# Kernel optimization log

Hardware: AMD Instinct MI355X
Metric: run time of the kernel (lower is better)

The kernel has to match this reference:

```python
import jax, jax.numpy as jnp
import numpy as np

N_NODES = 100000
N_EDGES = 1600000
IN_F, HID, OUT_F = 50, 256, 121


def setup_inputs() -> dict:
    key = jax.random.key(0)
    ks = jax.random.split(key, 8)
    x = jax.random.normal(ks[0], (N_NODES, IN_F), dtype=jnp.float32)
    edge_index = jax.random.randint(ks[1], (2, N_EDGES), 0, N_NODES, dtype=jnp.int64)
    W1 = jax.random.normal(ks[2], (IN_F, HID), dtype=jnp.float32) * (1.0 / np.sqrt(IN_F))
    b1 = jnp.zeros((HID,), dtype=jnp.float32)
    W2 = jax.random.normal(ks[3], (HID, HID), dtype=jnp.float32) * (1.0 / np.sqrt(HID))
    b2 = jnp.zeros((HID,), dtype=jnp.float32)
    W3 = jax.random.normal(ks[4], (HID, OUT_F), dtype=jnp.float32) * (1.0 / np.sqrt(HID))
    b3 = jnp.zeros((OUT_F,), dtype=jnp.float32)
    return {"x": x, "edge_index": edge_index, "W1": W1, "b1": b1,
            "W2": W2, "b2": b2, "W3": W3, "b3": b3}


def _gcn_norm(edge_index, num_nodes):
    # PyG gcn_norm: add self-loops, symmetric degree normalization.
    loop = jnp.arange(num_nodes, dtype=edge_index.dtype)
    row = jnp.concatenate([edge_index[0], loop])  # source
    col = jnp.concatenate([edge_index[1], loop])  # target (aggregation dim)
    ones = jnp.ones(row.shape[0], dtype=jnp.float32)
    deg = jax.ops.segment_sum(ones, col, num_segments=num_nodes)
    dinv = jnp.where(deg > 0, jax.lax.rsqrt(deg), 0.0)
    norm = dinv[row] * dinv[col]  # [E+N]
    return row, col, norm


def _gcn_conv(x, W, b, row, col, norm, num_nodes):
    h = x @ W                                   # [N, F_out] dense transform
    msg = h[row] * norm[:, None]                # gather + scale  [E+N, F_out]
    agg = jax.ops.segment_sum(msg, col, num_segments=num_nodes)  # scatter-add
    return agg + b


def reference(x, edge_index, W1, b1, W2, b2, W3, b3):
    n = x.shape[0]
    row, col, norm = _gcn_norm(edge_index, n)
    # layer 1 + relu (dropout is identity in eval mode)
    x1 = _gcn_conv(x, W1, b1, row, col, norm, n)
    h = jax.nn.relu(x1)
    # layer 2 + relu
    x1 = _gcn_conv(h, W2, b2, row, col, norm, n)
    h = jax.nn.relu(x1)
    # layer 3; module returns pre-relu output x1 of the last conv
    x1 = _gcn_conv(h, W3, b3, row, col, norm, n)
    return x1
```

## Files before the change

### kernel.cpp

```cpp
#include <hip/hip_runtime.h>


#define IN_F 50
#define HID  256
#define OUT_F 121
#define KP1  64
#define NP3  128
#define MPAD 100096

typedef __attribute__((ext_vector_type(8))) short bf16x8;
typedef __attribute__((ext_vector_type(4))) float f32x4;

__device__ __forceinline__ float bf2f(unsigned short u) {
    union { unsigned int i; float f; } x; x.i = ((unsigned int)u) << 16; return x.f;
}
__device__ __forceinline__ unsigned short f2bf(float f) {
    union { float f; unsigned int i; } x; x.f = f;
    unsigned int r = x.i + 0x7FFFu + ((x.i >> 16) & 1u);
    return (unsigned short)(r >> 16);
}

__device__ __forceinline__ void gl2lds16(const void* g, void* l) {
    __builtin_amdgcn_global_load_lds(
        (const __attribute__((address_space(1))) void*)g,
        (__attribute__((address_space(3))) void*)l, 16, 0, 0);
}

__global__ void k_detect(const int* __restrict__ ei, int* __restrict__ flag, int N) {
    int i = threadIdx.x;
    int lo = ei[2 * i], hi = ei[2 * i + 1];
    int bad = (hi != 0) || ((unsigned)lo >= (unsigned)N);
    unsigned long long m = __ballot(bad);
    if (threadIdx.x == 0) *flag = (m == 0ULL) ? 1 : 0;
}


__global__ void k_count(const int* __restrict__ ei, const int* __restrict__ flag,
                        int* __restrict__ cnt, int E, int N) {
    int t = blockIdx.x * blockDim.x + threadIdx.x;
    if (t >= E) return;
    int f = *flag;
    int c = f ? ei[2 * (E + t)] : ei[E + t];
    c = min(max(c, 0), N - 1);
    atomicAdd(&cnt[c], 1);
}

__global__ __launch_bounds__(1024) void k_scan(const int* __restrict__ cnt,
                                               int* __restrict__ offs,
                                               float* __restrict__ dinv, int n) {
    __shared__ int wsum[16];
    __shared__ int s_carry;
    int lane = threadIdx.x & 63, wid = threadIdx.x >> 6;
    if (threadIdx.x == 0) s_carry = 0;
    __syncthreads();
    for (int base = 0; base < n; base += 4096) {
        int i0 = base + (int)threadIdx.x * 4;
        int v0 = (i0 + 0 < n) ? cnt[i0 + 0] : 0;
        int v1 = (i0 + 1 < n) ? cnt[i0 + 1] : 0;
        int v2 = (i0 + 2 < n) ? cnt[i0 + 2] : 0;
        int v3 = (i0 + 3 < n) ? cnt[i0 + 3] : 0;
        int s1 = v0 + v1, s2 = s1 + v2, tsum = s2 + v3;
        int x = tsum;
        #pragma unroll
        for (int d = 1; d < 64; d <<= 1) {
            int y = __shfl_up(x, d, 64);
            if (lane >= d) x += y;
        }
        if (lane == 63) wsum[wid] = x;
        __syncthreads();
        int wpre = 0;
        #pragma unroll
        for (int j = 0; j < 16; j++) wpre += (j < wid) ? wsum[j] : 0;
        int carry = s_carry;
        int e0 = carry + wpre + x - tsum;
        if (i0 + 0 < n) { offs[i0+0]=e0;    dinv[i0+0]=rsqrtf((float)(v0+1)); }
        if (i0 + 1 < n) { offs[i0+1]=e0+v0; dinv[i0+1]=rsqrtf((float)(v1+1)); }
        if (i0 + 2 < n) { offs[i0+2]=e0+s1; dinv[i0+2]=rsqrtf((float)(v2+1)); }
        if (i0 + 3 < n) { offs[i0+3]=e0+s2; dinv[i0+3]=rsqrtf((float)(v3+1)); }
        __syncthreads();
        if (threadIdx.x == 1023) s_carry = carry + wpre + x;
        __syncthreads();
    }
    if (threadIdx.x == 0) offs[n] = s_carry;
}

__global__ void k_fill(const int* __restrict__ ei, const int* __restrict__ flag,
                       const int* __restrict__ offs,
                       int* __restrict__ fillc, int* __restrict__ rowidx, int E, int N) {
    int t = blockIdx.x * blockDim.x + threadIdx.x;
    if (t >= E) return;
    int f = *flag;
    int c = f ? ei[2 * (E + t)] : ei[E + t];
    int r = f ? ei[2 * t] : ei[t];
    c = min(max(c, 0), N - 1);
    r = min(max(r, 0), N - 1);
    int pos = offs[c] + atomicAdd(&fillc[c], 1);
    if ((unsigned)pos < (unsigned)E) rowidx[pos] = r;
}


__global__ void k_padx(const float* __restrict__ x, const float* __restrict__ dinv,
                       unsigned short* __restrict__ Xs, int N) {
    int idx = blockIdx.x * blockDim.x + threadIdx.x;
    if (idx >= N * KP1) return;
    int node = idx >> 6, k = idx & 63;
    Xs[idx] = (k < IN_F) ? f2bf(dinv[node] * x[node * IN_F + k]) : (unsigned short)0;
}

__global__ void k_tr(const float* __restrict__ W, unsigned short* __restrict__ Bt,
                     int K, int Nw, int Kp, int Np) {
    int idx = blockIdx.x * blockDim.x + threadIdx.x;
    if (idx >= Np * Kp) return;
    int nn = idx / Kp, k = idx - nn * Kp;
    Bt[idx] = (k < K && nn < Nw) ? f2bf(W[k * Nw + nn]) : (unsigned short)0;
}

__global__ __launch_bounds__(256) void k_gemm_lds(const unsigned short* __restrict__ A,
                                                  const unsigned short* __restrict__ Bt,
                                                  const float* __restrict__ dinv,
                                                  const float* __restrict__ bias,
                                                  unsigned short* __restrict__ C,
                                                  int K, int Nout,
                                                  int BIAS, int RELU, int SCALE) {
    __shared__ char lds[16384];
    const int tid = threadIdx.x;
    const int wid = tid >> 6, lane = tid & 63;
    const int wm = wid & 1, wn = wid >> 1;
    const int quad = lane >> 4, ml = lane & 15;
    const int m0 = blockIdx.x * 128;
    const int n0g = blockIdx.y * 128;

    f32x4 acc[4][4];
    #pragma unroll
    for (int a = 0; a < 4; a++)
        #pragma unroll
        for (int b = 0; b < 4; b++) acc[a][b] = (f32x4){0.f, 0.f, 0.f, 0.f};

    for (int kk = 0; kk < K; kk += 32) {
        #pragma unroll
        for (int r = 0; r < 2; r++) {
            int c = r * 256 + tid;
            int row = c >> 2, q = c & 3;
            gl2lds16(A  + (size_t)(m0  + row) * K + kk + q * 8, lds + c * 16);
            gl2lds16(Bt + (size_t)(n0g + row) * K + kk + q * 8, lds + 8192 + c * 16);
        }
        __syncthreads();
        bf16x8 af[4], bfv[4];
        #pragma unroll
        for (int mf = 0; mf < 4; mf++)
            af[mf] = *(const bf16x8*)(lds + ((wm * 64 + mf * 16 + ml) * 64 + quad * 16));
        #pragma unroll
        for (int nf = 0; nf < 4; nf++)
            bfv[nf] = *(const bf16x8*)(lds + 8192 + ((wn * 64 + nf * 16 + ml) * 64 + quad * 16));
        #pragma unroll
        for (int mf = 0; mf < 4; mf++)
            #pragma unroll
            for (int nf = 0; nf < 4; nf++)
                acc[mf][nf] = __builtin_amdgcn_mfma_f32_16x16x32_bf16(af[mf], bfv[nf], acc[mf][nf], 0, 0, 0);
        __syncthreads();
    }

    #pragma unroll
    for (int mf = 0; mf < 4; mf++) {
        int r0 = m0 + wm * 64 + mf * 16 + quad * 4;
        float dd[4] = {1.f, 1.f, 1.f, 1.f};
        if (SCALE) { dd[0]=dinv[r0]; dd[1]=dinv[r0+1]; dd[2]=dinv[r0+2]; dd[3]=dinv[r0+3]; }
        #pragma unroll
        for (int nf = 0; nf < 4; nf++) {
            int col = n0g + wn * 64 + nf * 16 + ml;
            float bb = BIAS ? bias[col] : 0.f;
            #pragma unroll
            for (int i = 0; i < 4; i++) {
                float v = acc[mf][nf][i] + bb;
                if (RELU) v = fmaxf(v, 0.f);
                v *= dd[i];
                C[(size_t)(r0 + i) * Nout + col] = f2bf(v);
            }
        }
    }
}


__device__ __forceinline__ int rclamp(int r, int N) { return min(max(r, 0), N - 1); }

__global__ void k_aggx(const unsigned short* __restrict__ Xs,
                       const int* __restrict__ offs, const int* __restrict__ rowidx,
                       const float* __restrict__ dinv, unsigned short* __restrict__ Y, int N) {
    int wid = threadIdx.x >> 6, lane = threadIdx.x & 63;
    int sub = lane >> 3, sl = lane & 7;
    int node = blockIdx.x * 32 + wid * 8 + sub;
    int nc = min(node, N - 1);
    int c = sl * 8;
    bf16x8 s = *(const bf16x8*)(Xs + (size_t)nc * KP1 + c);
    float a[8];
    #pragma unroll
    for (int k = 0; k < 8; k++) a[k] = bf2f((unsigned short)s[k]);
    int e = offs[nc], end = offs[nc + 1];
    if (node >= N) { e = 0; end = 0; }
    while (__any(e < end)) {
        int r[4]; float m[4];
        #pragma unroll
        for (int j = 0; j < 4; j++) {
            int idx = e + j;
            m[j] = (idx < end) ? 1.f : 0.f;
            idx = min(idx, end - 1); idx = max(idx, 0);
            r[j] = rclamp(rowidx[idx], N);
        }
        bf16x8 u[4];
        #pragma unroll
        for (int j = 0; j < 4; j++)
            u[j] = *(const bf16x8*)(Xs + (size_t)r[j] * KP1 + c);
        #pragma unroll
        for (int j = 0; j < 4; j++)
            #pragma unroll
            for (int k = 0; k < 8; k++)
                a[k] = fmaf(bf2f((unsigned short)u[j][k]), m[j], a[k]);
        e += 4;
    }
    if (node < N) {
        float dv = dinv[node];
        bf16x8 o;
        #pragma unroll
        for (int k = 0; k < 8; k++) o[k] = (short)f2bf(a[k] * dv);
        *(bf16x8*)(Y + (size_t)node * KP1 + c) = o;
    }
}

__global__ void k_agg256s(const unsigned short* __restrict__ Hn,
                          const int* __restrict__ offs, const int* __restrict__ rowidx,
                          const float* __restrict__ dinv, unsigned short* __restrict__ Y,
                          int N, int half_n) {
    int cell = blockIdx.x & 7;
    int chunk = cell >> 1, half = cell & 1;
    int idx = blockIdx.x >> 3;
    int wid = threadIdx.x >> 6, lane = threadIdx.x & 63;
    int sub = lane >> 3, sl = lane & 7;
    int node = half * half_n + idx * 32 + wid * 8 + sub;
    int hi_end = min((half + 1) * half_n, N);
    int ok = node < hi_end;
    int nc = ok ? node : hi_end - 1;
    int c = chunk * 64 + sl * 8;
    bf16x8 s = *(const bf16x8*)(Hn + (size_t)nc * HID + c);
    float a[8];
    #pragma unroll
    for (int k = 0; k < 8; k++) a[k] = bf2f((unsigned short)s[k]);
    int e = offs[nc], end = offs[nc + 1];
    if (!ok) { e = 0; end = 0; }
    while (__any(e < end)) {
        int r[4]; float m[4];
        #pragma unroll
        for (int j = 0; j < 4; j++) {
            int idx2 = e + j;
            m[j] = (idx2 < end) ? 1.f : 0.f;
            idx2 = min(idx2, end - 1); idx2 = max(idx2, 0);
            r[j] = rclamp(rowidx[idx2], N);
        }
        bf16x8 u[4];
        #pragma unroll
        for (int j = 0; j < 4; j++)
            u[j] = *(const bf16x8*)(Hn + (size_t)r[j] * HID + c);
        #pragma unroll
        for (int j = 0; j < 4; j++)
            #pragma unroll
            for (int k = 0; k < 8; k++)
                a[k] = fmaf(bf2f((unsigned short)u[j][k]), m[j], a[k]);
        e += 4;
    }
    if (ok) {
        float dv = dinv[node];
        bf16x8 o;
        #pragma unroll
        for (int k = 0; k < 8; k++) o[k] = (short)f2bf(a[k] * dv);
        *(bf16x8*)(Y + (size_t)node * HID + c) = o;
    }
}

__global__ void k_aggouts(const unsigned short* __restrict__ G,
                          const int* __restrict__ offs, const int* __restrict__ rowidx,
                          const float* __restrict__ dinv, const float* __restrict__ bias,
                          float* __restrict__ out, int N, int quar_n) {
    int cell = blockIdx.x & 7;
    int chunk = cell >> 2, quar = cell & 3;
    int idx = blockIdx.x >> 3;
    int wid = threadIdx.x >> 6, lane = threadIdx.x & 63;
    int sub = lane >> 3, sl = lane & 7;
    int node = quar * quar_n + idx * 32 + wid * 8 + sub;
    int hi_end = min((quar + 1) * quar_n, N);
    int ok = node < hi_end;
    int nc = ok ? node : hi_end - 1;
    int c = chunk * 64 + sl * 8;
    bf16x8 s = *(const bf16x8*)(G + (size_t)nc * NP3 + c);
    float a[8];
    #pragma unroll
    for (int k = 0; k < 8; k++) a[k] = bf2f((unsigned short)s[k]);
    int e = offs[nc], end = offs[nc + 1];
    if (!ok) { e = 0; end = 0; }
    while (__any(e < end)) {
        int r[4]; float m[4];
        #pragma unroll
        for (int j = 0; j < 4; j++) {
            int idx2 = e + j;
            m[j] = (idx2 < end) ? 1.f : 0.f;
            idx2 = min(idx2, end - 1); idx2 = max(idx2, 0);
            r[j] = rclamp(rowidx[idx2], N);
        }
        bf16x8 u[4];
        #pragma unroll
        for (int j = 0; j < 4; j++)
            u[j] = *(const bf16x8*)(G + (size_t)r[j] * NP3 + c);
        #pragma unroll
        for (int j = 0; j < 4; j++)
            #pragma unroll
            for (int k = 0; k < 8; k++)
                a[k] = fmaf(bf2f((unsigned short)u[j][k]), m[j], a[k]);
        e += 4;
    }
    if (ok) {
        float dv = dinv[node];
        #pragma unroll
        for (int k = 0; k < 8; k++) {
            int col = c + k;
            if (col < OUT_F)
                out[(size_t)node * OUT_F + col] = fmaf(a[k], dv, bias[col]);
        }
    }
}


extern "C" void kernel_launch(void* const* d_in, const int* in_sizes, int n_in,
                              void* d_out, int out_size, void* d_ws, size_t ws_size,
                              hipStream_t stream) {
    const float* x  = (const float*)d_in[0];
    const int*   ei = (const int*)d_in[1];
    const float* W1 = (const float*)d_in[2];
    const float* b1 = (const float*)d_in[3];
    const float* W2 = (const float*)d_in[4];
    const float* b2 = (const float*)d_in[5];
    const float* W3 = (const float*)d_in[6];
    const float* b3 = (const float*)d_in[7];
    float* out = (float*)d_out;

    const int N = in_sizes[0] / IN_F;
    const int E = in_sizes[1] / 2;

    char* w = (char*)d_ws;
    size_t off = 0;
    auto alloc = [&](size_t bytes) -> char* {
        char* p = w + off;
        off += (bytes + 255) & ~(size_t)255;
        return p;
    };
    int*   cnt    = (int*)  alloc((size_t)N * 4);
    int*   offs   = (int*)  alloc((size_t)(N + 1) * 4);
    int*   fillc  = (int*)  alloc((size_t)N * 4);
    float* dinv   = (float*)alloc((size_t)MPAD * 4);
    int*   flag   = (int*)  alloc(256);
    int*   rowidx = (int*)  alloc((size_t)E * 4);
    unsigned short* Bt1 = (unsigned short*)alloc((size_t)HID * KP1 * 2);
    unsigned short* Bt2 = (unsigned short*)alloc((size_t)HID * HID * 2);
    unsigned short* Bt3 = (unsigned short*)alloc((size_t)NP3 * HID * 2);
    unsigned short* bufA = (unsigned short*)alloc((size_t)MPAD * HID * 2);
    unsigned short* bufB = (unsigned short*)alloc((size_t)MPAD * HID * 2);
    unsigned short* Xs  = bufA;
    unsigned short* Y1  = bufB;
    unsigned short* H1s = bufA;
    unsigned short* Y2  = bufB;
    unsigned short* H2  = bufA;
    unsigned short* G3  = bufB;

    hipMemsetAsync(cnt, 0, (size_t)N * 4, stream);
    hipMemsetAsync(fillc, 0, (size_t)N * 4, stream);
    hipMemsetAsync(rowidx, 0, (size_t)E * 4, stream);

    k_detect<<<1, 64, 0, stream>>>(ei, flag, N);
    k_count<<<(E + 255) / 256, 256, 0, stream>>>(ei, flag, cnt, E, N);
    k_scan<<<1, 1024, 0, stream>>>(cnt, offs, dinv, N);
    k_fill<<<(E + 255) / 256, 256, 0, stream>>>(ei, flag, offs, fillc, rowidx, E, N);

    k_padx<<<(N * KP1 + 255) / 256, 256, 0, stream>>>(x, dinv, Xs, N);
    k_tr<<<(HID * KP1 + 255) / 256, 256, 0, stream>>>(W1, Bt1, IN_F, HID, KP1, HID);
    k_tr<<<(HID * HID + 255) / 256, 256, 0, stream>>>(W2, Bt2, HID, HID, HID, HID);
    k_tr<<<(NP3 * HID + 255) / 256, 256, 0, stream>>>(W3, Bt3, HID, OUT_F, HID, NP3);

    dim3 g12(MPAD / 128, HID / 128);
    dim3 g3(MPAD / 128, NP3 / 128);

    int half_n = (N + 1) / 2;
    int bpc2 = (half_n + 31) / 32;
    int quar_n = (N + 3) / 4;
    int bpc3 = (quar_n + 31) / 32;

    k_aggx<<<(N + 31) / 32, 256, 0, stream>>>(Xs, offs, rowidx, dinv, Y1, N);
    k_gemm_lds<<<g12, 256, 0, stream>>>(Y1, Bt1, dinv, b1, H1s, KP1, HID, 1, 1, 1);
    k_agg256s<<<8 * bpc2, 256, 0, stream>>>(H1s, offs, rowidx, dinv, Y2, N, half_n);
    k_gemm_lds<<<g12, 256, 0, stream>>>(Y2, Bt2, dinv, b2, H2, HID, HID, 1, 1, 0);
    k_gemm_lds<<<g3, 256, 0, stream>>>(H2, Bt3, dinv, b3, G3, HID, NP3, 0, 0, 1);
    k_aggouts<<<8 * bpc3, 256, 0, stream>>>(G3, offs, rowidx, dinv, b3, out, N, quar_n);

    (void)n_in; (void)out_size; (void)ws_size;
}
```

Before: 639.3 us.

## Fuse layer-2 and layer-3 GEMMs, merge prep kernels, retile aggregation kernels

Layer-2 GEMM (with bias and ReLU) and the layer-3 GEMM now run in one kernel. The intermediate H2 tile stays in swizzled LDS, so the 100k x 256 bf16 round trip through global memory is avoided. Input padding and the three weight transposes become one launch, and the three memsets collapse into one. The aggregation kernels move to 32-column chunks with 4 lanes per node, giving more nodes per wave and a different feature split. The fused kernel uses 64KB of LDS and large accumulator arrays, which may lower occupancy, and it reads B3 straight from global memory.

Result: slower. 834.8 us (+30.6%).

```diff
diff --git a/kernel.cpp b/kernel.cpp
--- a/kernel.cpp
+++ b/kernel.cpp
@@ -98,21 +98,42 @@
     if ((unsigned)pos < (unsigned)E) rowidx[pos] = r;
 }
 
-
-__global__ void k_padx(const float* __restrict__ x, const float* __restrict__ dinv,
-                       unsigned short* __restrict__ Xs, int N) {
-    int idx = blockIdx.x * blockDim.x + threadIdx.x;
-    if (idx >= N * KP1) return;
-    int node = idx >> 6, k = idx & 63;
-    Xs[idx] = (k < IN_F) ? f2bf(dinv[node] * x[node * IN_F + k]) : (unsigned short)0;
-}
-
-__global__ void k_tr(const float* __restrict__ W, unsigned short* __restrict__ Bt,
-                     int K, int Nw, int Kp, int Np) {
-    int idx = blockIdx.x * blockDim.x + threadIdx.x;
-    if (idx >= Np * Kp) return;
-    int nn = idx / Kp, k = idx - nn * Kp;
-    Bt[idx] = (k < K && nn < Nw) ? f2bf(W[k * Nw + nn]) : (unsigned short)0;
+__global__ void k_prep(const float* __restrict__ x, const float* __restrict__ dinv,
+                       unsigned short* __restrict__ Xs,
+                       const float* __restrict__ W1, unsigned short* __restrict__ Bt1,
+                       const float* __restrict__ W2, unsigned short* __restrict__ Bt2,
+                       const float* __restrict__ W3, unsigned short* __restrict__ Bt3,
+                       int N) {
+    int bid = blockIdx.x;
+    int npadx = (N * KP1 + 255) / 256;
+    if (bid < npadx) {
+        int idx = bid * 256 + (int)threadIdx.x;
+        if (idx < N * KP1) {
+            int node = idx >> 6, k = idx & 63;
+            Xs[idx] = (k < IN_F) ? f2bf(dinv[node] * x[node * IN_F + k]) : (unsigned short)0;
+        }
+        return;
+    }
+    bid -= npadx;
+    if (bid < (HID * KP1) / 256) {
+        int idx = bid * 256 + (int)threadIdx.x;
+        int nn = idx >> 6, k = idx & 63;
+        Bt1[idx] = (k < IN_F) ? f2bf(W1[k * HID + nn]) : (unsigned short)0;
+        return;
+    }
+    bid -= (HID * KP1) / 256;
+    if (bid < (HID * HID) / 256) {
+        int idx = bid * 256 + (int)threadIdx.x;
+        int nn = idx >> 8, k = idx & 255;
+        Bt2[idx] = f2bf(W2[k * HID + nn]);
+        return;
+    }
+    bid -= (HID * HID) / 256;
+    {
+        int idx = bid * 256 + (int)threadIdx.x;
+        int nn = idx >> 8, k = idx & 255;
+        Bt3[idx] = (nn < OUT_F) ? f2bf(W3[k * OUT_F + nn]) : (unsigned short)0;
+    }
 }
 
 __global__ __launch_bounds__(256) void k_gemm_lds(const unsigned short* __restrict__ A,
@@ -180,6 +201,108 @@
     }
 }
 
+__global__ __launch_bounds__(256) void k_mlp23(const unsigned short* __restrict__ A,
+                                               const unsigned short* __restrict__ B2t,
+                                               const unsigned short* __restrict__ B3t,
+                                               const float* __restrict__ b2,
+                                               const float* __restrict__ dinv,
+                                               unsigned short* __restrict__ G) {
+    __shared__ char lds[65536];
+    const int tid = threadIdx.x;
+    const int wid = tid >> 6, lane = tid & 63;
+    const int wm = wid & 1, wn = wid >> 1;
+    const int quad = lane >> 4, ml = lane & 15;
+    const int m0 = blockIdx.x * 128;
+
+    f32x4 acc1[4][8];
+    #pragma unroll
+    for (int a = 0; a < 4; a++)
+        #pragma unroll
+        for (int b = 0; b < 8; b++) acc1[a][b] = (f32x4){0.f, 0.f, 0.f, 0.f};
+
+    for (int kk = 0; kk < HID; kk += 32) {
+        #pragma unroll
+        for (int r = 0; r < 2; r++) {
+            int c = r * 256 + tid;
+            int row = c >> 2, q = c & 3;
+            gl2lds16(A + (size_t)(m0 + row) * HID + kk + q * 8, lds + c * 16);
+        }
+        #pragma unroll
+        for (int r = 0; r < 4; r++) {
+            int c = r * 256 + tid;
+            int nn = c >> 2, q = c & 3;
+            gl2lds16(B2t + (size_t)nn * HID + kk + q * 8, lds + 8192 + c * 16);
+        }
+        __syncthreads();
+        bf16x8 af[4], bv[8];
+        #pragma unroll
+        for (int mf = 0; mf < 4; mf++)
+            af[mf] = *(const bf16x8*)(lds + ((wm * 64 + mf * 16 + ml) * 64 + quad * 16));
+        #pragma unroll
+        for (int nf = 0; nf < 8; nf++)
+            bv[nf] = *(const bf16x8*)(lds + 8192 + ((wn * 128 + nf * 16 + ml) * 64 + quad * 16));
+        #pragma unroll
+        for (int mf = 0; mf < 4; mf++)
+            #pragma unroll
+            for (int nf = 0; nf < 8; nf++)
+                acc1[mf][nf] = __builtin_amdgcn_mfma_f32_16x16x32_bf16(af[mf], bv[nf], acc1[mf][nf], 0, 0, 0);
+        __syncthreads();
+    }
+
+    #pragma unroll
+    for (int nf = 0; nf < 8; nf++) {
+        int col = wn * 128 + nf * 16 + ml;
+        float bb = b2[col];
+        #pragma unroll
+        for (int mf = 0; mf < 4; mf++) {
+            int rl = wm * 64 + mf * 16 + quad * 4;
+            #pragma unroll
+            for (int i = 0; i < 4; i++) {
+                int row = rl + i;
+                int byte = (row * 512 + col * 2) ^ ((row & 7) << 4);
+                *(unsigned short*)(lds + byte) = f2bf(fmaxf(acc1[mf][nf][i] + bb, 0.f));
+            }
+        }
+    }
+    __syncthreads();
+
+    f32x4 acc2[4][4];
+    #pragma unroll
+    for (int a = 0; a < 4; a++)
+        #pragma unroll
+        for (int b = 0; b < 4; b++) acc2[a][b] = (f32x4){0.f, 0.f, 0.f, 0.f};
+
+    for (int kk = 0; kk < HID; kk += 32) {
+        bf16x8 af2[4], bv2[4];
+        #pragma unroll
+        for (int mf = 0; mf < 4; mf++) {
+            int row = wm * 64 + mf * 16 + ml;
+            int byte = (row * 512 + kk * 2 + quad * 16) ^ ((row & 7) << 4);
+            af2[mf] = *(const bf16x8*)(lds + byte);
+        }
+        #pragma unroll
+        for (int nf = 0; nf < 4; nf++)
+            bv2[nf] = *(const bf16x8*)(B3t + (size_t)(wn * 64 + nf * 16 + ml) * HID + kk + quad * 8);
+        #pragma unroll
+        for (int mf = 0; mf < 4; mf++)
+            #pragma unroll
+            for (int nf = 0; nf < 4; nf++)
+                acc2[mf][nf] = __builtin_amdgcn_mfma_f32_16x16x32_bf16(af2[mf], bv2[nf], acc2[mf][nf], 0, 0, 0);
+    }
+
+    #pragma unroll
+    for (int mf = 0; mf < 4; mf++) {
+        int r0 = m0 + wm * 64 + mf * 16 + quad * 4;
+        float dd[4] = {dinv[r0], dinv[r0+1], dinv[r0+2], dinv[r0+3]};
+        #pragma unroll
+        for (int nf = 0; nf < 4; nf++) {
+            int col = wn * 64 + nf * 16 + ml;
+            #pragma unroll
+            for (int i = 0; i < 4; i++)
+                G[(size_t)(r0 + i) * NP3 + col] = f2bf(acc2[mf][nf][i] * dd[i]);
+        }
+    }
+}
 
 __device__ __forceinline__ int rclamp(int r, int N) { return min(max(r, 0), N - 1); }
 
@@ -226,20 +349,18 @@
     }
 }
 
-__global__ void k_agg256s(const unsigned short* __restrict__ Hn,
+__global__ void k_agg256c(const unsigned short* __restrict__ Hn,
                           const int* __restrict__ offs, const int* __restrict__ rowidx,
                           const float* __restrict__ dinv, unsigned short* __restrict__ Y,
-                          int N, int half_n) {
-    int cell = blockIdx.x & 7;
-    int chunk = cell >> 1, half = cell & 1;
+                          int N) {
+    int chunk = blockIdx.x & 7;
     int idx = blockIdx.x >> 3;
     int wid = threadIdx.x >> 6, lane = threadIdx.x & 63;
-    int sub = lane >> 3, sl = lane & 7;
-    int node = half * half_n + idx * 32 + wid * 8 + sub;
-    int hi_end = min((half + 1) * half_n, N);
-    int ok = node < hi_end;
-    int nc = ok ? node : hi_end - 1;
-    int c = chunk * 64 + sl * 8;
+    int sub = lane >> 2, sl = lane & 3;
+    int node = idx * 64 + wid * 16 + sub;
+    int ok = node < N;
+    int nc = ok ? node : N - 1;
+    int c = chunk * 32 + sl * 8;
     bf16x8 s = *(const bf16x8*)(Hn + (size_t)nc * HID + c);
     float a[8];
     #pragma unroll
@@ -275,20 +396,20 @@
     }
 }
 
-__global__ void k_aggouts(const unsigned short* __restrict__ G,
-                          const int* __restrict__ offs, const int* __restrict__ rowidx,
-                          const float* __restrict__ dinv, const float* __restrict__ bias,
-                          float* __restrict__ out, int N, int quar_n) {
+__global__ void k_aggouts64(const unsigned short* __restrict__ G,
+                            const int* __restrict__ offs, const int* __restrict__ rowidx,
+                            const float* __restrict__ dinv, const float* __restrict__ bias,
+                            float* __restrict__ out, int N, int half_n) {
     int cell = blockIdx.x & 7;
-    int chunk = cell >> 2, quar = cell & 3;
+    int chunk = cell >> 1, half = cell & 1;
     int idx = blockIdx.x >> 3;
     int wid = threadIdx.x >> 6, lane = threadIdx.x & 63;
-    int sub = lane >> 3, sl = lane & 7;
-    int node = quar * quar_n + idx * 32 + wid * 8 + sub;
-    int hi_end = min((quar + 1) * quar_n, N);
+    int sub = lane >> 2, sl = lane & 3;
+    int node = half * half_n + idx * 64 + wid * 16 + sub;
+    int hi_end = min((half + 1) * half_n, N);
     int ok = node < hi_end;
     int nc = ok ? node : hi_end - 1;
-    int c = chunk * 64 + sl * 8;
+    int c = chunk * 32 + sl * 8;
     bf16x8 s = *(const bf16x8*)(G + (size_t)nc * NP3 + c);
     float a[8];
     #pragma unroll
@@ -351,8 +472,8 @@
         return p;
     };
     int*   cnt    = (int*)  alloc((size_t)N * 4);
+    int*   fillc  = (int*)  alloc((size_t)N * 4);
     int*   offs   = (int*)  alloc((size_t)(N + 1) * 4);
-    int*   fillc  = (int*)  alloc((size_t)N * 4);
     float* dinv   = (float*)alloc((size_t)MPAD * 4);
     int*   flag   = (int*)  alloc(256);
     int*   rowidx = (int*)  alloc((size_t)E * 4);
@@ -365,37 +486,28 @@
     unsigned short* Y1  = bufB;
     unsigned short* H1s = bufA;
     unsigned short* Y2  = bufB;
-    unsigned short* H2  = bufA;
-    unsigned short* G3  = bufB;
-
-    hipMemsetAsync(cnt, 0, (size_t)N * 4, stream);
-    hipMemsetAsync(fillc, 0, (size_t)N * 4, stream);
-    hipMemsetAsync(rowidx, 0, (size_t)E * 4, stream);
+    unsigned short* G3  = bufA;
+
+    size_t msz = (size_t)((char*)fillc - (char*)cnt) + (size_t)N * 4;
+    hipMemsetAsync(cnt, 0, msz, stream);
 
     k_detect<<<1, 64, 0, stream>>>(ei, flag, N);
     k_count<<<(E + 255) / 256, 256, 0, stream>>>(ei, flag, cnt, E, N);
     k_scan<<<1, 1024, 0, stream>>>(cnt, offs, dinv, N);
     k_fill<<<(E + 255) / 256, 256, 0, stream>>>(ei, flag, offs, fillc, rowidx, E, N);
 
-    k_padx<<<(N * KP1 + 255) / 256, 256, 0, stream>>>(x, dinv, Xs, N);
-    k_tr<<<(HID * KP1 + 255) / 256, 256, 0, stream>>>(W1, Bt1, IN_F, HID, KP1, HID);
-    k_tr<<<(HID * HID + 255) / 256, 256, 0, stream>>>(W2, Bt2, HID, HID, HID, HID);
-    k_tr<<<(NP3 * HID + 255) / 256, 256, 0, stream>>>(W3, Bt3, HID, OUT_F, HID, NP3);
-
-    dim3 g12(MPAD / 128, HID / 128);
-    dim3 g3(MPAD / 128, NP3 / 128);
-
+    int prep_grid = (N * KP1 + 255) / 256 + (HID * KP1) / 256 + (HID * HID) / 256 + (NP3 * HID) / 256;
+    k_prep<<<prep_grid, 256, 0, stream>>>(x, dinv, Xs, W1, Bt1, W2, Bt2, W3, Bt3, N);
+
+    k_aggx<<<(N + 31) / 32, 256, 0, stream>>>(Xs, offs, rowidx, dinv, Y1, N);
+    dim3 g1(MPAD / 128, HID / 128);
+    k_gemm_lds<<<g1, 256, 0, stream>>>(Y1, Bt1, dinv, b1, H1s, KP1, HID, 1, 1, 1);
+    int bpc2 = (N + 63) / 64;
+    k_agg256c<<<8 * bpc2, 256, 0, stream>>>(H1s, offs, rowidx, dinv, Y2, N);
+    k_mlp23<<<MPAD / 128, 256, 0, stream>>>(Y2, Bt2, Bt3, b2, dinv, G3);
     int half_n = (N + 1) / 2;
-    int bpc2 = (half_n + 31) / 32;
-    int quar_n = (N + 3) / 4;
-    int bpc3 = (quar_n + 31) / 32;
-
-    k_aggx<<<(N + 31) / 32, 256, 0, stream>>>(Xs, offs, rowidx, dinv, Y1, N);
-    k_gemm_lds<<<g12, 256, 0, stream>>>(Y1, Bt1, dinv, b1, H1s, KP1, HID, 1, 1, 1);
-    k_agg256s<<<8 * bpc2, 256, 0, stream>>>(H1s, offs, rowidx, dinv, Y2, N, half_n);
-    k_gemm_lds<<<g12, 256, 0, stream>>>(Y2, Bt2, dinv, b2, H2, HID, HID, 1, 1, 0);
-    k_gemm_lds<<<g3, 256, 0, stream>>>(H2, Bt3, dinv, b3, G3, HID, NP3, 0, 0, 1);
-    k_aggouts<<<8 * bpc3, 256, 0, stream>>>(G3, offs, rowidx, dinv, b3, out, N, quar_n);
+    int bpc3 = (half_n + 63) / 64;
+    k_aggouts64<<<8 * bpc3, 256, 0, stream>>>(G3, offs, rowidx, dinv, b3, out, N, half_n);
 
     (void)n_in; (void)out_size; (void)ws_size;
 }
```
